# Performance work log

Hardware: AMD Instinct MI355X
Metric: run time of the kernel (lower is better)

Reference implementation:

```python
import jax, jax.numpy as jnp
import numpy as np

T, B, F, H = 128, 64, 75, 512
J = F  # attention dim == number of input features (joints)


def _lstm_dir(x, h0, c0, Wih, Whh, bih, bhh, reverse):
    # x: (T,B,Fin). Precompute input projection once (big GEMM), scan the recurrence.
    xw = jnp.einsum('tbf,gf->tbg', x, Wih) + bih + bhh  # (T,B,4H)

    def step(carry, xt):
        h, c = carry
        g = xt + h @ Whh.T  # (B,4H), PyTorch gate order i,f,g,o
        i, f, gg, o = jnp.split(g, 4, axis=-1)
        c = jax.nn.sigmoid(f) * c + jax.nn.sigmoid(i) * jnp.tanh(gg)
        h = jax.nn.sigmoid(o) * jnp.tanh(c)
        return (h, c), h

    (hT, cT), ys = jax.lax.scan(step, (h0, c0), xw, reverse=reverse)
    return ys, hT


def _bilstm(x, h0, c0, Wih, Whh, bih, bhh):
    # params have leading direction axis of size 2
    yf, hf = _lstm_dir(x, h0[0], c0[0], Wih[0], Whh[0], bih[0], bhh[0], False)
    yb, hb = _lstm_dir(x, h0[1], c0[1], Wih[1], Whh[1], bih[1], bhh[1], True)
    return jnp.concatenate([yf, yb], axis=-1), jnp.stack([hf, hb])


def setup_inputs() -> dict:
    key = jax.random.key(0)
    ks = iter(jax.random.split(key, 40))

    def p(*shape):
        return (jax.random.normal(next(ks), shape, dtype=jnp.float32) * 0.05)

    inp = {
        'x': jax.random.normal(next(ks), (T, B, F), dtype=jnp.float32),
        'h0': jnp.zeros((6, B, H), jnp.float32),
        'c0': jnp.zeros((6, B, H), jnp.float32),
        # salstm: 1-layer bidirectional, input F
        'sa_Wih': p(2, 4 * H, F), 'sa_Whh': p(2, 4 * H, H),
        'sa_bih': p(2, 4 * H), 'sa_bhh': p(2, 4 * H),
        # mainlstm layer 0 (input F)
        'm0_Wih': p(2, 4 * H, F), 'm0_Whh': p(2, 4 * H, H),
        'm0_bih': p(2, 4 * H), 'm0_bhh': p(2, 4 * H),
        # mainlstm layers 1,2 (input 2H), stacked on leading layer axis
        'mL_Wih': p(2, 2, 4 * H, 2 * H), 'mL_Whh': p(2, 2, 4 * H, H),
        'mL_bih': p(2, 2, 4 * H), 'mL_bhh': p(2, 2, 4 * H),
        'safc1_W': p(H, H), 'safc1_b': p(H),
        'safc2_W': p(J, H), 'safc2_b': p(J),
        'fc1_W': p(H, 2 * H), 'fc1_b': p(H),
    }
    return inp


def reference(x, h0, c0, sa_Wih, sa_Whh, sa_bih, sa_bhh,
              m0_Wih, m0_Whh, m0_bih, m0_bhh,
              mL_Wih, mL_Whh, mL_bih, mL_bhh,
              safc1_W, safc1_b, safc2_W, safc2_b, fc1_W, fc1_b):
    # spatial-attention LSTM
    sa_out, sa_hn = _bilstm(x, h0[:2], c0[:2], sa_Wih, sa_Whh, sa_bih, sa_bhh)  # sa_hn (2,B,H)
    e = jnp.exp(jnp.tanh(sa_hn @ safc1_W.T + safc1_b) @ safc2_W.T + safc2_b)  # (2,B,J)
    alpha = e / e.sum(axis=(0, 2), keepdims=True)  # per-batch normalization
    # replace all weights >= 0.1 with their selected mean (per batch element)
    mask = alpha >= 0.1
    cnt = mask.sum(axis=(0, 2), keepdims=True)
    sel_mean = (alpha * mask).sum(axis=(0, 2), keepdims=True) / jnp.maximum(cnt, 1)
    alpha = jnp.where(mask, sel_mean, alpha)
    alpha_b = alpha.mean(axis=0)  # (B,J) -- reconcile direction axis for broadcast

    xw = x * alpha_b[None]  # (T,B,F)

    # 3-layer bidirectional main LSTM
    y, _ = _bilstm(xw, h0[0:2], c0[0:2], m0_Wih, m0_Whh, m0_bih, m0_bhh)
    for l in range(2):
        y, _ = _bilstm(y, h0[2 + 2 * l:4 + 2 * l], c0[2 + 2 * l:4 + 2 * l],
                       mL_Wih[l], mL_Whh[l], mL_bih[l], mL_bhh[l])
    out = y @ fc1_W.T + fc1_b  # (T,B,H)
    return out
```

## Files before the change

### kernel.cpp

```cpp
#include <hip/hip_runtime.h>
#include <cstddef>

#define T_  128
#define B_  64
#define F_  75
#define H_  512
#define G4_ 2048
#define TB_ (T_ * B_)
#define KP_ 128

typedef __bf16 bf16x8 __attribute__((ext_vector_type(8)));
typedef float  f32x4  __attribute__((ext_vector_type(4)));
typedef unsigned long long u64;
typedef unsigned long long __attribute__((may_alias)) u64a;

__device__ __forceinline__ short f2b(float x) {
    union { float f; unsigned u; } v; v.f = x;
    return (short)((v.u + 0x7fffu + ((v.u >> 16) & 1u)) >> 16);
}
__device__ __forceinline__ float b2f(short s) {
    union { float f; unsigned u; } v; v.u = ((unsigned)(unsigned short)s) << 16;
    return v.f;
}
__device__ __forceinline__ void gload16(const void* g, void* l) {
    __builtin_amdgcn_global_load_lds(
        (const __attribute__((address_space(1))) void*)g,
        (__attribute__((address_space(3))) void*)l, 16, 0, 0);
}
__device__ __forceinline__ float fsig(float x) {
    return __builtin_amdgcn_rcpf(1.f + __expf(-x));
}
__device__ __forceinline__ float ftanh(float x) {
    return 1.f - 2.f * __builtin_amdgcn_rcpf(1.f + __expf(2.f * x));
}

__global__ __launch_bounds__(256) void gemm_bf16(
    const short* __restrict__ A, const short* __restrict__ Bm,
    float* __restrict__ C, float* __restrict__ P, int M, int N, int K,
    const float* __restrict__ bias1, const float* __restrict__ bias2)
{
    __shared__ short As[4096];
    __shared__ short Bs[4096];
    const int tid = threadIdx.x;
    const int m_base = blockIdx.y * 128;
    const int n_base = blockIdx.x * 128;
    const int w = tid >> 6, lane = tid & 63;
    const int wm = (w >> 1) * 64, wn = (w & 1) * 64;
    const int lm = lane & 15, q = lane >> 4;

    f32x4 acc[4][4];
#pragma unroll
    for (int i = 0; i < 4; i++)
#pragma unroll
        for (int j = 0; j < 4; j++)
#pragma unroll
            for (int r = 0; r < 4; r++) acc[i][j][r] = 0.f;

    const int s0 = tid, s1 = tid + 256;
    const int r0 = s0 & 127, c0 = s0 >> 7;
    const int r1 = s1 & 127, c1 = s1 >> 7;

    for (int k0 = 0; k0 < K; k0 += 32) {
        __syncthreads();
        gload16(A + (size_t)(m_base + r0) * K + k0 + c0 * 8, &As[s0 * 8]);
        gload16(A + (size_t)(m_base + r1) * K + k0 + c1 * 8, &As[s1 * 8]);
        gload16(Bm + (size_t)(n_base + r0) * K + k0 + c0 * 8, &Bs[s0 * 8]);
        gload16(Bm + (size_t)(n_base + r1) * K + k0 + c1 * 8, &Bs[s1 * 8]);
        __syncthreads();
        bf16x8 af[4], bfv[4];
#pragma unroll
        for (int i = 0; i < 4; i++) {
            af[i]  = *(const bf16x8*)&As[((q * 128) + wm + i * 16 + lm) * 8];
            bfv[i] = *(const bf16x8*)&Bs[((q * 128) + wn + i * 16 + lm) * 8];
        }
#pragma unroll
        for (int i = 0; i < 4; i++)
#pragma unroll
            for (int j = 0; j < 4; j++)
                acc[i][j] = __builtin_amdgcn_mfma_f32_16x16x32_bf16(
                    af[i], bfv[j], acc[i][j], 0, 0, 0);
    }

#pragma unroll
    for (int i = 0; i < 4; i++) {
#pragma unroll
        for (int j = 0; j < 4; j++) {
            const int gm0 = m_base + wm + i * 16 + q * 4;
            const int gn = n_base + wn + j * 16 + lm;
            float bb = (bias1 ? bias1[gn] : 0.f) + (bias2 ? bias2[gn] : 0.f);
            if (P) {
                const int g = gn >> 9, u = gn & 511;
                const int ub = u >> 4, lmu = u & 15;
#pragma unroll
                for (int r = 0; r < 4; r++) {
                    const int gm = gm0 + r;
                    const int t = gm >> 6, b = gm & 63;
                    const int tidS = (b >> 4) * 64 + ((b >> 2) & 3) * 16 + lmu;
                    size_t idx = ((((size_t)t * 32 + ub) * 4 + (b & 3)) * 256 + tidS) * 4 + g;
                    P[idx] = acc[i][j][r] + bb;
                }
            } else {
#pragma unroll
                for (int r = 0; r < 4; r++)
                    C[(size_t)(gm0 + r) * N + gn] = acc[i][j][r] + bb;
            }
        }
    }
}

__global__ __launch_bounds__(256) void pack_whh(
    const float* __restrict__ W, short* __restrict__ Wpk)
{
    int i = blockIdx.x * 256 + threadIdx.x;
    if (i >= 2 * G4_ * H_) return;
    int e = i & 7, lane = (i >> 3) & 63, it = (i >> 9) & 15;
    int g = (i >> 13) & 3, ub = (i >> 15) & 31, dir = (i >> 20) & 1;
    int lm = lane & 15, qq = lane >> 4;
    float v = W[((size_t)dir * G4_ + g * H_ + ub * 16 + lm) * H_
                + it * 32 + qq * 8 + e];
    Wpk[i] = f2b(v);
}

__global__ __launch_bounds__(256) void init_phase(
    const float* __restrict__ h0s, short* __restrict__ Ht,
    unsigned* __restrict__ bar, int zero_bar)
{
    int i = blockIdx.x * 256 + threadIdx.x;
    if (i < 2 * B_ * H_) Ht[i] = f2b(h0s[i]);
    if (zero_bar && i < 64) bar[i] = 0;
}

__global__ __launch_bounds__(256) void prep_init(
    const float* __restrict__ h0, short* __restrict__ HtA,
    short* __restrict__ HtB, short* __restrict__ HtC, short* __restrict__ HtD,
    unsigned* __restrict__ bar)
{
    int i = blockIdx.x * 256 + threadIdx.x;
    if (i < 2 * B_ * H_) {
        short vA = f2b(h0[i]);
        HtA[i] = vA;
        HtB[i] = vA;
        HtC[i] = f2b(h0[2 * B_ * H_ + i]);
        HtD[i] = f2b(h0[4 * B_ * H_ + i]);
    }
    if (i < 64) bar[i] = 0;
}

__global__ __launch_bounds__(256) void ht_to_f32(
    const short* __restrict__ Ht0, float* __restrict__ out)
{
    int i = blockIdx.x * 256 + threadIdx.x;
    if (i < 2 * B_ * H_) out[i] = b2f(Ht0[i]);
}

__global__ __launch_bounds__(256, 1) void lstm_phase(
    const float* __restrict__ XW,
    const short* __restrict__ Wpk,
    short* __restrict__ Ht,
    const float* __restrict__ c0p,
    short* __restrict__ Y,
    unsigned* __restrict__ bar, int phase,
    const short* __restrict__ jA, const short* __restrict__ jB,
    float* __restrict__ jP, float* __restrict__ jC,
    const float* __restrict__ jb1, const float* __restrict__ jb2, int job)
{
    __shared__ short Ws[32768];
    __shared__ short Tb[64 * 24];
    __shared__ unsigned arrv;
    const int tid = threadIdx.x, w = tid >> 6, lane = tid & 63;
    const int lm = lane & 15, q = lane >> 4;

    if (blockIdx.x >= 32) {
        if (job == 0) return;
        short* As = Ws;
        short* Bs = Ws + 4096;
        const int hh = blockIdx.x - 32;
        const int dirh = blockIdx.y;
        const unsigned pT = (unsigned)(phase * T_);
        const int wm = (w >> 1) * 64, wn = (w & 1) * 64;

        const short* Bop; float* Pd; float* Cd; const float* b1; const float* b2;
        int n_tile, grp, iters, stride;
        if (job == 1) {
            Bop = jB + (size_t)dirh * G4_ * 1024;
            Pd = jP + (size_t)dirh * TB_ * G4_;
            Cd = nullptr;
            b1 = jb1 + dirh * G4_; b2 = jb2 + dirh * G4_;
            n_tile = hh & 15; grp = hh >> 4; iters = 16; stride = 4;
        } else {
            Bop = jB; Pd = nullptr; Cd = jC; b1 = jb1; b2 = nullptr;
            int H2 = dirh * 64 + hh;
            n_tile = H2 & 3; grp = H2 >> 2; iters = 2; stride = 32;
        }
        const int n_base = n_tile * 128;

        for (int it2 = 0; it2 < iters; it2++) {
            int j = grp + stride * it2;
            int k = (j & 1) ? 32 + (j >> 1) : 31 - (j >> 1);
            int m_base = k * 128, t0 = 2 * k;
            if (w == 0) {
                unsigned tgt = (lane < 32) ? pT + (unsigned)(t0 + 2)
                                           : pT + (unsigned)(T_ - t0);
                int itc = 0;
                for (;;) {
                    unsigned v = __hip_atomic_load(&bar[lane], __ATOMIC_RELAXED,
                                                   __HIP_MEMORY_SCOPE_AGENT);
                    if (__all(v >= tgt)) break;
                    if (++itc > (1 << 19)) break;
                    __builtin_amdgcn_s_sleep(32);
                }
            }
            __syncthreads();

            f32x4 acc[4][4];
#pragma unroll
            for (int i = 0; i < 4; i++)
#pragma unroll
                for (int jj = 0; jj < 4; jj++)
#pragma unroll
                    for (int r = 0; r < 4; r++) acc[i][jj][r] = 0.f;

            const int s0 = tid, s1 = tid + 256;
            const int r0 = s0 & 127, cc0 = s0 >> 7;
            const int r1 = s1 & 127, cc1 = s1 >> 7;
            for (int k0 = 0; k0 < 1024; k0 += 32) {
                __syncthreads();
                gload16(jA + (size_t)(m_base + r0) * 1024 + k0 + cc0 * 8, &As[s0 * 8]);
                gload16(jA + (size_t)(m_base + r1) * 1024 + k0 + cc1 * 8, &As[s1 * 8]);
                gload16(Bop + (size_t)(n_base + r0) * 1024 + k0 + cc0 * 8, &Bs[s0 * 8]);
                gload16(Bop + (size_t)(n_base + r1) * 1024 + k0 + cc1 * 8, &Bs[s1 * 8]);
                __syncthreads();
                bf16x8 af[4], bfv[4];
#pragma unroll
                for (int i = 0; i < 4; i++) {
                    af[i]  = *(const bf16x8*)&As[((q * 128) + wm + i * 16 + lm) * 8];
                    bfv[i] = *(const bf16x8*)&Bs[((q * 128) + wn + i * 16 + lm) * 8];
                }
#pragma unroll
                for (int i = 0; i < 4; i++)
#pragma unroll
                    for (int jj = 0; jj < 4; jj++)
                        acc[i][jj] = __builtin_amdgcn_mfma_f32_16x16x32_bf16(
                            af[i], bfv[jj], acc[i][jj], 0, 0, 0);
            }
#pragma unroll
            for (int i = 0; i < 4; i++) {
#pragma unroll
                for (int jj = 0; jj < 4; jj++) {
                    const int gm0 = m_base + wm + i * 16 + q * 4;
                    const int gn = n_base + wn + jj * 16 + lm;
                    float bb = b1[gn] + (b2 ? b2[gn] : 0.f);
                    if (Pd) {
                        const int g = gn >> 9, u = gn & 511;
                        const int ub2 = u >> 4, lmu = u & 15;
#pragma unroll
                        for (int r = 0; r < 4; r++) {
                            const int gm = gm0 + r;
                            const int t = gm >> 6, b = gm & 63;
                            const int tidS = (b >> 4) * 64 + ((b >> 2) & 3) * 16 + lmu;
                            size_t idx = ((((size_t)t * 32 + ub2) * 4 + (b & 3)) * 256 + tidS) * 4 + g;
                            Pd[idx] = acc[i][jj][r] + bb;
                        }
                    } else {
#pragma unroll
                        for (int r = 0; r < 4; r++)
                            Cd[(size_t)(gm0 + r) * 512 + gn] = acc[i][jj][r] + bb;
                    }
                }
            }
        }
        return;
    }

    const int dir = blockIdx.y, ub = blockIdx.x, u0 = ub * 16;
    if (tid == 0) arrv = 0;

    const short* wsrc = Wpk + (size_t)(dir * 32 + ub) * 32768;
#pragma unroll
    for (int p = 0; p < 16; p++)
        gload16(wsrc + (tid + 256 * p) * 8, &Ws[(tid + 256 * p) * 8]);

    const int b0 = w * 16 + q * 4;
    const int u = u0 + lm;
    unsigned* slots = bar + dir * 32;

    float c[4];
    f32x4 xw[4];
#pragma unroll
    for (int r = 0; r < 4; r++)
        c[r] = c0p[(size_t)dir * B_ * H_ + (size_t)(b0 + r) * H_ + u];
    {
        const int t0 = dir ? (T_ - 1) : 0;
        const float* xp = XW + ((size_t)dir * T_ + t0) * (B_ * G4_) + (size_t)ub * 4096;
#pragma unroll
        for (int r = 0; r < 4; r++)
            xw[r] = *(const f32x4*)(xp + r * 1024 + tid * 4);
    }
    __syncthreads();

    for (int s = 0; s < T_; s++) {
        const int t = dir ? (T_ - 1 - s) : s;
        const short* Hc = Ht + ((size_t)((s & 1) * 2 + dir) << 15);

        u64 hq[32];
        const short* hrow = Hc + (w * 16 + lm) * 512 + q * 8;
#pragma unroll
        for (int it = 0; it < 16; it++) {
            const u64* hp = (const u64*)(hrow + it * 32);
            hq[2 * it]     = __hip_atomic_load((u64*)hp,     __ATOMIC_RELAXED, __HIP_MEMORY_SCOPE_AGENT);
            hq[2 * it + 1] = __hip_atomic_load((u64*)hp + 1, __ATOMIC_RELAXED, __HIP_MEMORY_SCOPE_AGENT);
        }

        f32x4 acc[4];
#pragma unroll
        for (int g = 0; g < 4; g++)
#pragma unroll
            for (int r = 0; r < 4; r++) acc[g][r] = 0.f;

#pragma unroll
        for (int it = 0; it < 16; it++) {
            union { u64 q2[2]; bf16x8 v; } ua;
            ua.q2[0] = hq[2 * it]; ua.q2[1] = hq[2 * it + 1];
#pragma unroll
            for (int g = 0; g < 4; g++) {
                bf16x8 bv = *(const bf16x8*)&Ws[((g * 16 + it) * 64 + lane) * 8];
                acc[g] = __builtin_amdgcn_mfma_f32_16x16x32_bf16(ua.v, bv, acc[g], 0, 0, 0);
            }
        }

#pragma unroll
        for (int r = 0; r < 4; r++) {
            float gi = acc[0][r] + xw[r][0];
            float gf = acc[1][r] + xw[r][1];
            float gg = acc[2][r] + xw[r][2];
            float go = acc[3][r] + xw[r][3];
            float cc = fsig(gf) * c[r] + fsig(gi) * ftanh(gg);
            c[r] = cc;
            Tb[(b0 + r) * 24 + lm] = f2b(fsig(go) * ftanh(cc));
        }
        __asm__ volatile("" ::: "memory");

        const int b = tid >> 2, qd = tid & 3;
        u64 v0 = *(const u64a*)&Tb[b * 24 + qd * 4];
        u64* ydst = Y ? (u64*)(Y + ((size_t)t * B_ + b) * (2 * H_) + dir * H_ + u0 + qd * 4)
                      : nullptr;
        {
            short* Hn = Ht + ((size_t)(((s + 1) & 1) * 2 + dir) << 15);
            __hip_atomic_store((u64*)(Hn + b * 512 + u0 + qd * 4), v0,
                               __ATOMIC_RELAXED, __HIP_MEMORY_SCOPE_AGENT);
        }
        if (ydst && job)
            __hip_atomic_store(ydst, v0, __ATOMIC_RELAXED, __HIP_MEMORY_SCOPE_AGENT);
        __asm__ volatile("s_waitcnt vmcnt(0)" ::: "memory");
        if (lane == 0)
            __hip_atomic_fetch_add(&arrv, 1u, __ATOMIC_RELAXED,
                                   __HIP_MEMORY_SCOPE_WORKGROUP);

        const unsigned tgt = (unsigned)(phase * T_ + s + 1);
        if (w == 0) {
            const unsigned a4 = 4u * (unsigned)(s + 1);
            while (__hip_atomic_load(&arrv, __ATOMIC_RELAXED,
                                     __HIP_MEMORY_SCOPE_WORKGROUP) < a4) {}
            if (lane == 0)
                __hip_atomic_store(&slots[ub], tgt,
                                   __ATOMIC_RELAXED, __HIP_MEMORY_SCOPE_AGENT);
        }

        if (ydst && !job) *(u64a*)ydst = v0;
        if (s < T_ - 1) {
            const int tn = dir ? (T_ - 2 - s) : (s + 1);
            const float* xp = XW + ((size_t)dir * T_ + tn) * (B_ * G4_) + (size_t)ub * 4096;
#pragma unroll
            for (int r = 0; r < 4; r++)
                xw[r] = *(const f32x4*)(xp + r * 1024 + tid * 4);

            if (w == 0) {
                unsigned v;
                for (;;) {
                    v = (lane < 32)
                        ? __hip_atomic_load(&slots[lane], __ATOMIC_RELAXED, __HIP_MEMORY_SCOPE_AGENT)
                        : tgt;
                    if (__all(v >= tgt)) break;
                    __builtin_amdgcn_s_sleep(1);
                }
            }
            __syncthreads();
        }
    }
}

__global__ __launch_bounds__(256) void gemm_bt(
    const float* __restrict__ A, const float* __restrict__ Bm,
    float* __restrict__ C, int M, int N, int K,
    const float* __restrict__ bias1, int act)
{
    __shared__ float As[16][68];
    __shared__ float Bs[16][68];
    const int tid = threadIdx.x;
    const int m_base = blockIdx.y * 64;
    const int n_base = blockIdx.x * 64;
    const int tm = tid >> 4, tn = tid & 15;
    float acc[4][4] = {};

    for (int k0 = 0; k0 < K; k0 += 16) {
#pragma unroll
        for (int i = 0; i < 4; i++) {
            int idx = tid * 4 + i;
            int r = idx >> 4, kk = idx & 15;
            int gm = m_base + r, gk = k0 + kk;
            As[kk][r] = (gm < M && gk < K) ? A[(size_t)gm * K + gk] : 0.f;
            int gn = n_base + r;
            Bs[kk][r] = (gn < N && gk < K) ? Bm[(size_t)gn * K + gk] : 0.f;
        }
        __syncthreads();
#pragma unroll
        for (int kk = 0; kk < 16; kk++) {
            float4 av = *(const float4*)&As[kk][tm * 4];
            float4 bv = *(const float4*)&Bs[kk][tn * 4];
            float a[4] = {av.x, av.y, av.z, av.w};
            float b[4] = {bv.x, bv.y, bv.z, bv.w};
#pragma unroll
            for (int i = 0; i < 4; i++)
#pragma unroll
                for (int j = 0; j < 4; j++)
                    acc[i][j] = fmaf(a[i], b[j], acc[i][j]);
        }
        __syncthreads();
    }
#pragma unroll
    for (int i = 0; i < 4; i++) {
        int gm = m_base + tm * 4 + i;
        if (gm >= M) continue;
#pragma unroll
        for (int j = 0; j < 4; j++) {
            int gn = n_base + tn * 4 + j;
            if (gn >= N) continue;
            float v = acc[i][j];
            if (bias1) v += bias1[gn];
            if (act == 1) v = tanhf(v);
            else if (act == 2) v = expf(v);
            C[(size_t)gm * N + gn] = v;
        }
    }
}

__global__ __launch_bounds__(256) void conv_f2b(
    const float* __restrict__ src, short* __restrict__ dst, int n)
{
    int i = blockIdx.x * 256 + threadIdx.x;
    if (i < n) dst[i] = f2b(src[i]);
}
__global__ __launch_bounds__(256) void conv_f2b_pad(
    const float* __restrict__ src, short* __restrict__ dst,
    int rows, int kin, int kp)
{
    int i = blockIdx.x * 256 + threadIdx.x;
    if (i < rows * kp) {
        int r = i / kp, k = i % kp;
        dst[i] = (k < kin) ? f2b(src[(size_t)r * kin + k]) : (short)0;
    }
}

__global__ __launch_bounds__(256) void attn_alpha(
    const float* __restrict__ E, float* __restrict__ AB)
{
    const int b = blockIdx.x, tid = threadIdx.x;
    __shared__ float red[256];
    __shared__ float adj[152];
    float v = 0.f;
    if (tid < 150) {
        int d = tid / F_, j = tid % F_;
        v = E[((size_t)d * B_ + b) * F_ + j];
    }
    red[tid] = v; __syncthreads();
    for (int s2 = 128; s2 > 0; s2 >>= 1) {
        if (tid < s2) red[tid] += red[tid + s2];
        __syncthreads();
    }
    float total = red[0]; __syncthreads();
    float alpha = v / total;
    float m = (tid < 150 && alpha >= 0.1f) ? 1.f : 0.f;
    red[tid] = m; __syncthreads();
    for (int s2 = 128; s2 > 0; s2 >>= 1) {
        if (tid < s2) red[tid] += red[tid + s2];
        __syncthreads();
    }
    float cnt = red[0]; __syncthreads();
    red[tid] = m * alpha; __syncthreads();
    for (int s2 = 128; s2 > 0; s2 >>= 1) {
        if (tid < s2) red[tid] += red[tid + s2];
        __syncthreads();
    }
    float selsum = red[0]; __syncthreads();
    float selmean = selsum / fmaxf(cnt, 1.f);
    if (tid < 150) adj[tid] = (m > 0.f) ? selmean : alpha;
    __syncthreads();
    if (tid < F_) AB[(size_t)b * F_ + tid] = 0.5f * (adj[tid] + adj[F_ + tid]);
}

__global__ __launch_bounds__(256) void scale_xb(
    const float* __restrict__ x, const float* __restrict__ AB,
    short* __restrict__ xb)
{
    int i = blockIdx.x * 256 + threadIdx.x;
    if (i < TB_ * KP_) {
        int r = i >> 7, k = i & 127;
        if (k < F_) {
            int b = r % B_;
            xb[i] = f2b(x[(size_t)r * F_ + k] * AB[(size_t)b * F_ + k]);
        } else xb[i] = 0;
    }
}

extern "C" void kernel_launch(void* const* d_in, const int* in_sizes, int n_in,
                              void* d_out, int out_size, void* d_ws, size_t ws_size,
                              hipStream_t stream)
{
    (void)in_sizes; (void)n_in; (void)out_size;
    const float* x       = (const float*)d_in[0];
    const float* h0      = (const float*)d_in[1];
    const float* c0      = (const float*)d_in[2];
    const float* sa_Wih  = (const float*)d_in[3];
    const float* sa_Whh  = (const float*)d_in[4];
    const float* sa_bih  = (const float*)d_in[5];
    const float* sa_bhh  = (const float*)d_in[6];
    const float* m0_Wih  = (const float*)d_in[7];
    const float* m0_Whh  = (const float*)d_in[8];
    const float* m0_bih  = (const float*)d_in[9];
    const float* m0_bhh  = (const float*)d_in[10];
    const float* mL_Wih  = (const float*)d_in[11];
    const float* mL_Whh  = (const float*)d_in[12];
    const float* mL_bih  = (const float*)d_in[13];
    const float* mL_bhh  = (const float*)d_in[14];
    const float* safc1_W = (const float*)d_in[15];
    const float* safc1_b = (const float*)d_in[16];
    const float* safc2_W = (const float*)d_in[17];
    const float* safc2_b = (const float*)d_in[18];
    const float* fc1_W   = (const float*)d_in[19];
    const float* fc1_b   = (const float*)d_in[20];

    char* cur = (char*)d_ws;
    auto alloc = [&](size_t bytes) {
        char* p = cur; cur += (bytes + 255) & ~(size_t)255; return p;
    };
    auto cv = [&](const float* s, short* d, int n) {
        conv_f2b<<<(n + 255) / 256, 256, 0, stream>>>(s, d, n);
    };

    const bool OV = ws_size >= 370000000ull;

    if (OV) {
        float*    XWa  = (float*)alloc((size_t)2 * TB_ * G4_ * 4);
        float*    XWb  = (float*)alloc((size_t)2 * TB_ * G4_ * 4);
        float*    T1b  = (float*)alloc(2 * B_ * H_ * 4);
        float*    Eb   = (float*)alloc(2 * B_ * F_ * 4);
        float*    AB   = (float*)alloc(B_ * F_ * 4);
        float*    saHf = (float*)alloc(2 * B_ * H_ * 4);
        short*    xb   = (short*)alloc((size_t)TB_ * KP_ * 2);
        short*    Y0b  = (short*)alloc((size_t)TB_ * 2 * H_ * 2);
        short*    Y1b  = (short*)alloc((size_t)TB_ * 2 * H_ * 2);
        short*    Y2b  = (short*)alloc((size_t)TB_ * 2 * H_ * 2);
        short*    HtA  = (short*)alloc((size_t)2 * 2 * B_ * H_ * 2);
        short*    HtB  = (short*)alloc((size_t)2 * 2 * B_ * H_ * 2);
        short*    HtC  = (short*)alloc((size_t)2 * 2 * B_ * H_ * 2);
        short*    HtD  = (short*)alloc((size_t)2 * 2 * B_ * H_ * 2);
        const size_t PK = (size_t)2 * G4_ * H_;
        short*    Wpk4 = (short*)alloc(4 * PK * 2);
        short*    WihbSA = (short*)alloc((size_t)2 * G4_ * KP_ * 2);
        short*    WihbM0 = (short*)alloc((size_t)2 * G4_ * KP_ * 2);
        short*    WihbL  = (short*)alloc((size_t)2 * 2 * G4_ * 2 * H_ * 2);
        short*    fc1b   = (short*)alloc((size_t)H_ * 2 * H_ * 2);
        unsigned* bar    = (unsigned*)alloc(1024);

        auto g16 = [&](const short* Ap, const short* Bp, float* Pp,
                       int K, const float* b1, const float* b2) {
            gemm_bf16<<<dim3(G4_ / 128, TB_ / 128), 256, 0, stream>>>(
                Ap, Bp, nullptr, Pp, TB_, G4_, K, b1, b2);
        };
        auto lstm = [&](const float* XWp, const short* Wp, short* Htp,
                        const float* c0p, short* Yp, int pidx,
                        const short* ja, const short* jb, float* jp, float* jc,
                        const float* b1, const float* b2, int job) {
            lstm_phase<<<dim3(job ? 96 : 32, 2), 256, 0, stream>>>(
                XWp, Wp, Htp, c0p, Yp, bar, pidx, ja, jb, jp, jc, b1, b2, job);
        };

        prep_init<<<256, 256, 0, stream>>>(h0, HtA, HtB, HtC, HtD, bar);
        cv(fc1_W, fc1b, H_ * 2 * H_);
        conv_f2b_pad<<<(2 * G4_ * KP_ + 255) / 256, 256, 0, stream>>>(sa_Wih, WihbSA, 2 * G4_, F_, KP_);
        conv_f2b_pad<<<(2 * G4_ * KP_ + 255) / 256, 256, 0, stream>>>(m0_Wih, WihbM0, 2 * G4_, F_, KP_);
        cv(mL_Wih, WihbL, 2 * 2 * G4_ * 2 * H_);
        pack_whh<<<(2 * G4_ * H_ + 255) / 256, 256, 0, stream>>>(sa_Whh, Wpk4);
        pack_whh<<<(2 * G4_ * H_ + 255) / 256, 256, 0, stream>>>(m0_Whh, Wpk4 + PK);
        pack_whh<<<(2 * G4_ * H_ + 255) / 256, 256, 0, stream>>>(mL_Whh, Wpk4 + 2 * PK);
        pack_whh<<<(2 * G4_ * H_ + 255) / 256, 256, 0, stream>>>(mL_Whh + (size_t)2 * G4_ * H_, Wpk4 + 3 * PK);
        conv_f2b_pad<<<(TB_ * KP_ + 255) / 256, 256, 0, stream>>>(x, xb, TB_, F_, KP_);

        for (int d = 0; d < 2; d++)
            g16(xb, WihbSA + (size_t)d * G4_ * KP_, XWa + (size_t)d * TB_ * G4_,
                KP_, sa_bih + d * G4_, sa_bhh + d * G4_);
        lstm(XWa, Wpk4, HtA, c0, nullptr, 0,
             nullptr, nullptr, nullptr, nullptr, nullptr, nullptr, 0);
        ht_to_f32<<<256, 256, 0, stream>>>(HtA, saHf);
        gemm_bt<<<dim3(8, 2), 256, 0, stream>>>(saHf, safc1_W, T1b, 2 * B_, H_, H_, safc1_b, 1);
        gemm_bt<<<dim3(2, 2), 256, 0, stream>>>(T1b, safc2_W, Eb, 2 * B_, F_, H_, safc2_b, 2);
        attn_alpha<<<B_, 256, 0, stream>>>(Eb, AB);
        scale_xb<<<(TB_ * KP_ + 255) / 256, 256, 0, stream>>>(x, AB, xb);

        for (int d = 0; d < 2; d++)
            g16(xb, WihbM0 + (size_t)d * G4_ * KP_, XWa + (size_t)d * TB_ * G4_,
                KP_, m0_bih + d * G4_, m0_bhh + d * G4_);
        lstm(XWa, Wpk4 + PK, HtB, c0, Y0b, 1,
             Y0b, WihbL, XWb, nullptr, mL_bih, mL_bhh, 1);

        lstm(XWb, Wpk4 + 2 * PK, HtC, c0 + 2 * B_ * H_, Y1b, 2,
             Y1b, WihbL + (size_t)2 * G4_ * 2 * H_, XWa, nullptr,
             mL_bih + 2 * G4_, mL_bhh + 2 * G4_, 1);

        lstm(XWa, Wpk4 + 3 * PK, HtD, c0 + 4 * B_ * H_, Y2b, 3,
             Y2b, fc1b, nullptr, (float*)d_out, fc1_b, nullptr, 2);
        return;
    }

    float*    XW   = (float*)alloc((size_t)2 * TB_ * G4_ * 4);
    float*    T1b  = (float*)alloc(2 * B_ * H_ * 4);
    float*    Eb   = (float*)alloc(2 * B_ * F_ * 4);
    float*    AB   = (float*)alloc(B_ * F_ * 4);
    float*    saHf = (float*)alloc(2 * B_ * H_ * 4);
    short*    xb   = (short*)alloc((size_t)TB_ * KP_ * 2);
    short*    Y0b  = (short*)alloc((size_t)TB_ * 2 * H_ * 2);
    short*    Y1b  = (short*)alloc((size_t)TB_ * 2 * H_ * 2);
    short*    Ht   = (short*)alloc((size_t)2 * 2 * B_ * H_ * 2);
    short*    Wpk  = (short*)alloc((size_t)2 * G4_ * H_ * 2);
    short*    Wihb = (short*)alloc((size_t)2 * G4_ * KP_ * 2);
    short*    WihbL= (short*)alloc((size_t)2 * G4_ * 2 * H_ * 2);
    short*    fc1b = (short*)alloc((size_t)H_ * 2 * H_ * 2);
    unsigned* bar  = (unsigned*)alloc(1024);

    auto g16f = [&](const short* Ap, const short* Bp, float* Cp, float* Pp,
                    int M, int N, int K, const float* b1, const float* b2) {
        gemm_bf16<<<dim3(N / 128, M / 128), 256, 0, stream>>>(Ap, Bp, Cp, Pp, M, N, K, b1, b2);
    };
    auto phase = [&](const float* Whh_p, const float* h0p, const float* c0p,
                     short* Yout, int pidx) {
        pack_whh<<<(2 * G4_ * H_ + 255) / 256, 256, 0, stream>>>(Whh_p, Wpk);
        init_phase<<<256, 256, 0, stream>>>(h0p, Ht, bar, pidx == 0 ? 1 : 0);
        lstm_phase<<<dim3(32, 2), 256, 0, stream>>>(XW, Wpk, Ht, c0p, Yout, bar, pidx,
            nullptr, nullptr, nullptr, nullptr, nullptr, nullptr, 0);
    };

    cv(fc1_W, fc1b, H_ * 2 * H_);
    conv_f2b_pad<<<(TB_ * KP_ + 255) / 256, 256, 0, stream>>>(x, xb, TB_, F_, KP_);
    conv_f2b_pad<<<(2 * G4_ * KP_ + 255) / 256, 256, 0, stream>>>(sa_Wih, Wihb, 2 * G4_, F_, KP_);
    for (int d = 0; d < 2; d++)
        g16f(xb, Wihb + (size_t)d * G4_ * KP_, nullptr, XW + (size_t)d * TB_ * G4_,
             TB_, G4_, KP_, sa_bih + d * G4_, sa_bhh + d * G4_);
    phase(sa_Whh, h0, c0, nullptr, 0);
    ht_to_f32<<<256, 256, 0, stream>>>(Ht, saHf);
    gemm_bt<<<dim3(8, 2), 256, 0, stream>>>(saHf, safc1_W, T1b, 2 * B_, H_, H_, safc1_b, 1);
    gemm_bt<<<dim3(2, 2), 256, 0, stream>>>(T1b, safc2_W, Eb, 2 * B_, F_, H_, safc2_b, 2);
    attn_alpha<<<B_, 256, 0, stream>>>(Eb, AB);
    scale_xb<<<(TB_ * KP_ + 255) / 256, 256, 0, stream>>>(x, AB, xb);

    conv_f2b_pad<<<(2 * G4_ * KP_ + 255) / 256, 256, 0, stream>>>(m0_Wih, Wihb, 2 * G4_, F_, KP_);
    for (int d = 0; d < 2; d++)
        g16f(xb, Wihb + (size_t)d * G4_ * KP_, nullptr, XW + (size_t)d * TB_ * G4_,
             TB_, G4_, KP_, m0_bih + d * G4_, m0_bhh + d * G4_);
    phase(m0_Whh, h0, c0, Y0b, 1);

    cv(mL_Wih, WihbL, 2 * G4_ * 2 * H_);
    for (int d = 0; d < 2; d++)
        g16f(Y0b, WihbL + (size_t)d * G4_ * 2 * H_, nullptr, XW + (size_t)d * TB_ * G4_,
             TB_, G4_, 2 * H_, mL_bih + d * G4_, mL_bhh + d * G4_);
    phase(mL_Whh, h0 + 2 * B_ * H_, c0 + 2 * B_ * H_, Y1b, 2);

    cv(mL_Wih + (size_t)2 * G4_ * 2 * H_, WihbL, 2 * G4_ * 2 * H_);
    for (int d = 0; d < 2; d++)
        g16f(Y1b, WihbL + (size_t)d * G4_ * 2 * H_, nullptr, XW + (size_t)d * TB_ * G4_,
             TB_, G4_, 2 * H_, mL_bih + (2 + d) * G4_, mL_bhh + (2 + d) * G4_);
    phase(mL_Whh + (size_t)2 * G4_ * H_, h0 + 4 * B_ * H_, c0 + 4 * B_ * H_, Y0b, 3);

    g16f(Y0b, fc1b, (float*)d_out, nullptr, TB_, H_, 2 * H_, fc1_b, nullptr);
}
```

Measured before the change: 4.144 ms.

## Store input-projection buffers in bf16 and shrink workspace to enable overlap path

The precomputed input-gate projections (XW) are now written as bf16 instead of fp32, and the LSTM recurrence loads and widens them to float per step. This halves the per-step global read traffic on the serial critical path. The smaller footprint lets the overlapped path (fused next-layer GEMM inside the recurrence kernel) fit in a much smaller workspace, so it is taken whenever space allows instead of only for a very large workspace. The cost is extra bf16 rounding of the projections and re-packing of weights between phases, since only one packed Whh buffer is kept.

Result: faster. 4.042 ms (-2.5%).

```diff
diff --git a/kernel.cpp b/kernel.cpp
--- a/kernel.cpp
+++ b/kernel.cpp
@@ -33,10 +33,19 @@
 __device__ __forceinline__ float ftanh(float x) {
     return 1.f - 2.f * __builtin_amdgcn_rcpf(1.f + __expf(2.f * x));
 }
+__device__ __forceinline__ f32x4 xw4(const short* xp) {
+    u64 v = *(const u64a*)xp;
+    f32x4 o;
+    o[0] = b2f((short)(v & 0xFFFFu));
+    o[1] = b2f((short)((v >> 16) & 0xFFFFu));
+    o[2] = b2f((short)((v >> 32) & 0xFFFFu));
+    o[3] = b2f((short)(v >> 48));
+    return o;
+}
 
 __global__ __launch_bounds__(256) void gemm_bf16(
     const short* __restrict__ A, const short* __restrict__ Bm,
-    float* __restrict__ C, float* __restrict__ P, int M, int N, int K,
+    float* __restrict__ C, short* __restrict__ P, int M, int N, int K,
     const float* __restrict__ bias1, const float* __restrict__ bias2)
 {
     __shared__ short As[4096];
@@ -97,7 +106,7 @@
                     const int t = gm >> 6, b = gm & 63;
                     const int tidS = (b >> 4) * 64 + ((b >> 2) & 3) * 16 + lmu;
                     size_t idx = ((((size_t)t * 32 + ub) * 4 + (b & 3)) * 256 + tidS) * 4 + g;
-                    P[idx] = acc[i][j][r] + bb;
+                    P[idx] = f2b(acc[i][j][r] + bb);
                 }
             } else {
 #pragma unroll
@@ -154,14 +163,14 @@
 }
 
 __global__ __launch_bounds__(256, 1) void lstm_phase(
-    const float* __restrict__ XW,
+    const short* __restrict__ XW,
     const short* __restrict__ Wpk,
     short* __restrict__ Ht,
     const float* __restrict__ c0p,
     short* __restrict__ Y,
     unsigned* __restrict__ bar, int phase,
     const short* __restrict__ jA, const short* __restrict__ jB,
-    float* __restrict__ jP, float* __restrict__ jC,
+    short* __restrict__ jP, float* __restrict__ jC,
     const float* __restrict__ jb1, const float* __restrict__ jb2, int job)
 {
     __shared__ short Ws[32768];
@@ -179,7 +188,7 @@
         const unsigned pT = (unsigned)(phase * T_);
         const int wm = (w >> 1) * 64, wn = (w & 1) * 64;
 
-        const short* Bop; float* Pd; float* Cd; const float* b1; const float* b2;
+        const short* Bop; short* Pd; float* Cd; const float* b1; const float* b2;
         int n_tile, grp, iters, stride;
         if (job == 1) {
             Bop = jB + (size_t)dirh * G4_ * 1024;
@@ -259,7 +268,7 @@
                             const int t = gm >> 6, b = gm & 63;
                             const int tidS = (b >> 4) * 64 + ((b >> 2) & 3) * 16 + lmu;
                             size_t idx = ((((size_t)t * 32 + ub2) * 4 + (b & 3)) * 256 + tidS) * 4 + g;
-                            Pd[idx] = acc[i][jj][r] + bb;
+                            Pd[idx] = f2b(acc[i][jj][r] + bb);
                         }
                     } else {
 #pragma unroll
@@ -291,10 +300,10 @@
         c[r] = c0p[(size_t)dir * B_ * H_ + (size_t)(b0 + r) * H_ + u];
     {
         const int t0 = dir ? (T_ - 1) : 0;
-        const float* xp = XW + ((size_t)dir * T_ + t0) * (B_ * G4_) + (size_t)ub * 4096;
+        const short* xp = XW + ((size_t)dir * T_ + t0) * (size_t)(B_ * G4_) + (size_t)ub * 4096;
 #pragma unroll
         for (int r = 0; r < 4; r++)
-            xw[r] = *(const f32x4*)(xp + r * 1024 + tid * 4);
+            xw[r] = xw4(xp + r * 1024 + tid * 4);
     }
     __syncthreads();
 
@@ -369,10 +378,10 @@
         if (ydst && !job) *(u64a*)ydst = v0;
         if (s < T_ - 1) {
             const int tn = dir ? (T_ - 2 - s) : (s + 1);
-            const float* xp = XW + ((size_t)dir * T_ + tn) * (B_ * G4_) + (size_t)ub * 4096;
+            const short* xp = XW + ((size_t)dir * T_ + tn) * (size_t)(B_ * G4_) + (size_t)ub * 4096;
 #pragma unroll
             for (int r = 0; r < 4; r++)
-                xw[r] = *(const f32x4*)(xp + r * 1024 + tid * 4);
+                xw[r] = xw4(xp + r * 1024 + tid * 4);
 
             if (w == 0) {
                 unsigned v;
@@ -539,7 +548,8 @@
     const float* fc1_W   = (const float*)d_in[19];
     const float* fc1_b   = (const float*)d_in[20];
 
-    char* cur = (char*)d_ws;
+    char* const start = (char*)d_ws;
+    char* cur = start;
     auto alloc = [&](size_t bytes) {
         char* p = cur; cur += (bytes + 255) & ~(size_t)255; return p;
     };
@@ -547,39 +557,34 @@
         conv_f2b<<<(n + 255) / 256, 256, 0, stream>>>(s, d, n);
     };
 
-    const bool OV = ws_size >= 370000000ull;
-
-    if (OV) {
-        float*    XWa  = (float*)alloc((size_t)2 * TB_ * G4_ * 4);
-        float*    XWb  = (float*)alloc((size_t)2 * TB_ * G4_ * 4);
-        float*    T1b  = (float*)alloc(2 * B_ * H_ * 4);
-        float*    Eb   = (float*)alloc(2 * B_ * F_ * 4);
-        float*    AB   = (float*)alloc(B_ * F_ * 4);
-        float*    saHf = (float*)alloc(2 * B_ * H_ * 4);
-        short*    xb   = (short*)alloc((size_t)TB_ * KP_ * 2);
-        short*    Y0b  = (short*)alloc((size_t)TB_ * 2 * H_ * 2);
-        short*    Y1b  = (short*)alloc((size_t)TB_ * 2 * H_ * 2);
-        short*    Y2b  = (short*)alloc((size_t)TB_ * 2 * H_ * 2);
-        short*    HtA  = (short*)alloc((size_t)2 * 2 * B_ * H_ * 2);
-        short*    HtB  = (short*)alloc((size_t)2 * 2 * B_ * H_ * 2);
-        short*    HtC  = (short*)alloc((size_t)2 * 2 * B_ * H_ * 2);
-        short*    HtD  = (short*)alloc((size_t)2 * 2 * B_ * H_ * 2);
-        const size_t PK = (size_t)2 * G4_ * H_;
-        short*    Wpk4 = (short*)alloc(4 * PK * 2);
-        short*    WihbSA = (short*)alloc((size_t)2 * G4_ * KP_ * 2);
-        short*    WihbM0 = (short*)alloc((size_t)2 * G4_ * KP_ * 2);
-        short*    WihbL  = (short*)alloc((size_t)2 * 2 * G4_ * 2 * H_ * 2);
-        short*    fc1b   = (short*)alloc((size_t)H_ * 2 * H_ * 2);
-        unsigned* bar    = (unsigned*)alloc(1024);
-
-        auto g16 = [&](const short* Ap, const short* Bp, float* Pp,
+    short*    XWa  = (short*)alloc((size_t)2 * TB_ * G4_ * 2);
+    short*    XWc  = (short*)alloc((size_t)2 * TB_ * G4_ * 2);
+    short*    Y0b  = (short*)alloc((size_t)TB_ * 2 * H_ * 2);
+    short*    Y1b  = (short*)alloc((size_t)TB_ * 2 * H_ * 2);
+    short*    Wpk  = (short*)alloc((size_t)2 * G4_ * H_ * 2);
+    short*    Wihb = (short*)alloc((size_t)2 * G4_ * KP_ * 2);
+    short*    WihbL= (short*)alloc((size_t)2 * G4_ * 2 * H_ * 2);
+    short*    fc1b = (short*)alloc((size_t)H_ * 2 * H_ * 2);
+    short*    xb   = (short*)alloc((size_t)TB_ * KP_ * 2);
+    float*    T1b  = (float*)alloc(2 * B_ * H_ * 4);
+    float*    Eb   = (float*)alloc(2 * B_ * F_ * 4);
+    float*    AB   = (float*)alloc(B_ * F_ * 4);
+    float*    saHf = (float*)alloc(2 * B_ * H_ * 4);
+    short*    HtA  = (short*)alloc((size_t)2 * 2 * B_ * H_ * 2);
+    short*    HtB  = (short*)alloc((size_t)2 * 2 * B_ * H_ * 2);
+    short*    HtC  = (short*)alloc((size_t)2 * 2 * B_ * H_ * 2);
+    short*    HtD  = (short*)alloc((size_t)2 * 2 * B_ * H_ * 2);
+    unsigned* bar  = (unsigned*)alloc(1024);
+
+    if ((size_t)(cur - start) <= ws_size) {
+        auto g16 = [&](const short* Ap, const short* Bp, short* Pp,
                        int K, const float* b1, const float* b2) {
             gemm_bf16<<<dim3(G4_ / 128, TB_ / 128), 256, 0, stream>>>(
                 Ap, Bp, nullptr, Pp, TB_, G4_, K, b1, b2);
         };
-        auto lstm = [&](const float* XWp, const short* Wp, short* Htp,
+        auto lstm = [&](const short* XWp, const short* Wp, short* Htp,
                         const float* c0p, short* Yp, int pidx,
-                        const short* ja, const short* jb, float* jp, float* jc,
+                        const short* ja, const short* jb, short* jp, float* jc,
                         const float* b1, const float* b2, int job) {
             lstm_phase<<<dim3(job ? 96 : 32, 2), 256, 0, stream>>>(
                 XWp, Wp, Htp, c0p, Yp, bar, pidx, ja, jb, jp, jc, b1, b2, job);
@@ -587,19 +592,15 @@
 
         prep_init<<<256, 256, 0, stream>>>(h0, HtA, HtB, HtC, HtD, bar);
         cv(fc1_W, fc1b, H_ * 2 * H_);
-        conv_f2b_pad<<<(2 * G4_ * KP_ + 255) / 256, 256, 0, stream>>>(sa_Wih, WihbSA, 2 * G4_, F_, KP_);
-        conv_f2b_pad<<<(2 * G4_ * KP_ + 255) / 256, 256, 0, stream>>>(m0_Wih, WihbM0, 2 * G4_, F_, KP_);
-        cv(mL_Wih, WihbL, 2 * 2 * G4_ * 2 * H_);
-        pack_whh<<<(2 * G4_ * H_ + 255) / 256, 256, 0, stream>>>(sa_Whh, Wpk4);
-        pack_whh<<<(2 * G4_ * H_ + 255) / 256, 256, 0, stream>>>(m0_Whh, Wpk4 + PK);
-        pack_whh<<<(2 * G4_ * H_ + 255) / 256, 256, 0, stream>>>(mL_Whh, Wpk4 + 2 * PK);
-        pack_whh<<<(2 * G4_ * H_ + 255) / 256, 256, 0, stream>>>(mL_Whh + (size_t)2 * G4_ * H_, Wpk4 + 3 * PK);
+        cv(mL_Wih, WihbL, 2 * G4_ * 2 * H_);
+        conv_f2b_pad<<<(2 * G4_ * KP_ + 255) / 256, 256, 0, stream>>>(sa_Wih, Wihb, 2 * G4_, F_, KP_);
         conv_f2b_pad<<<(TB_ * KP_ + 255) / 256, 256, 0, stream>>>(x, xb, TB_, F_, KP_);
+        pack_whh<<<(2 * G4_ * H_ + 255) / 256, 256, 0, stream>>>(sa_Whh, Wpk);
 
         for (int d = 0; d < 2; d++)
-            g16(xb, WihbSA + (size_t)d * G4_ * KP_, XWa + (size_t)d * TB_ * G4_,
+            g16(xb, Wihb + (size_t)d * G4_ * KP_, XWa + (size_t)d * TB_ * G4_,
                 KP_, sa_bih + d * G4_, sa_bhh + d * G4_);
-        lstm(XWa, Wpk4, HtA, c0, nullptr, 0,
+        lstm(XWa, Wpk, HtA, c0, nullptr, 0,
              nullptr, nullptr, nullptr, nullptr, nullptr, nullptr, 0);
         ht_to_f32<<<256, 256, 0, stream>>>(HtA, saHf);
         gemm_bt<<<dim3(8, 2), 256, 0, stream>>>(saHf, safc1_W, T1b, 2 * B_, H_, H_, safc1_b, 1);
@@ -607,78 +608,83 @@
         attn_alpha<<<B_, 256, 0, stream>>>(Eb, AB);
         scale_xb<<<(TB_ * KP_ + 255) / 256, 256, 0, stream>>>(x, AB, xb);
 
+        conv_f2b_pad<<<(2 * G4_ * KP_ + 255) / 256, 256, 0, stream>>>(m0_Wih, Wihb, 2 * G4_, F_, KP_);
         for (int d = 0; d < 2; d++)
-            g16(xb, WihbM0 + (size_t)d * G4_ * KP_, XWa + (size_t)d * TB_ * G4_,
+            g16(xb, Wihb + (size_t)d * G4_ * KP_, XWa + (size_t)d * TB_ * G4_,
                 KP_, m0_bih + d * G4_, m0_bhh + d * G4_);
-        lstm(XWa, Wpk4 + PK, HtB, c0, Y0b, 1,
-             Y0b, WihbL, XWb, nullptr, mL_bih, mL_bhh, 1);
-
-        lstm(XWb, Wpk4 + 2 * PK, HtC, c0 + 2 * B_ * H_, Y1b, 2,
-             Y1b, WihbL + (size_t)2 * G4_ * 2 * H_, XWa, nullptr,
-             mL_bih + 2 * G4_, mL_bhh + 2 * G4_, 1);
-
-        lstm(XWa, Wpk4 + 3 * PK, HtD, c0 + 4 * B_ * H_, Y2b, 3,
-             Y2b, fc1b, nullptr, (float*)d_out, fc1_b, nullptr, 2);
+        pack_whh<<<(2 * G4_ * H_ + 255) / 256, 256, 0, stream>>>(m0_Whh, Wpk);
+        lstm(XWa, Wpk, HtB, c0, Y0b, 1,
+             Y0b, WihbL, XWc, nullptr, mL_bih, mL_bhh, 1);
+
+        cv(mL_Wih + (size_t)2 * G4_ * 2 * H_, WihbL, 2 * G4_ * 2 * H_);
+        pack_whh<<<(2 * G4_ * H_ + 255) / 256, 256, 0, stream>>>(mL_Whh, Wpk);
+        lstm(XWc, Wpk, HtC, c0 + 2 * B_ * H_, Y1b, 2,
+             Y1b, WihbL, XWa, nullptr, mL_bih + 2 * G4_, mL_bhh + 2 * G4_, 1);
+
+        pack_whh<<<(2 * G4_ * H_ + 255) / 256, 256, 0, stream>>>(mL_Whh + (size_t)2 * G4_ * H_, Wpk);
+        lstm(XWa, Wpk, HtD, c0 + 4 * B_ * H_, Y0b, 3,
+             Y0b, fc1b, nullptr, (float*)d_out, fc1_b, nullptr, 2);
         return;
     }
 
-    float*    XW   = (float*)alloc((size_t)2 * TB_ * G4_ * 4);
-    float*    T1b  = (float*)alloc(2 * B_ * H_ * 4);
-    float*    Eb   = (float*)alloc(2 * B_ * F_ * 4);
-    float*    AB   = (float*)alloc(B_ * F_ * 4);
-    float*    saHf = (float*)alloc(2 * B_ * H_ * 4);
-    short*    xb   = (short*)alloc((size_t)TB_ * KP_ * 2);
-    short*    Y0b  = (short*)alloc((size_t)TB_ * 2 * H_ * 2);
-    short*    Y1b  = (short*)alloc((size_t)TB_ * 2 * H_ * 2);
-    short*    Ht   = (short*)alloc((size_t)2 * 2 * B_ * H_ * 2);
-    short*    Wpk  = (short*)alloc((size_t)2 * G4_ * H_ * 2);
-    short*    Wihb = (short*)alloc((size_t)2 * G4_ * KP_ * 2);
-    short*    WihbL= (short*)alloc((size_t)2 * G4_ * 2 * H_ * 2);
-    short*    fc1b = (short*)alloc((size_t)H_ * 2 * H_ * 2);
-    unsigned* bar  = (unsigned*)alloc(1024);
-
-    auto g16f = [&](const short* Ap, const short* Bp, float* Cp, float* Pp,
+    cur = start;
+    short*    XW    = (short*)alloc((size_t)2 * TB_ * G4_ * 2);
+    float*    T1f   = (float*)alloc(2 * B_ * H_ * 4);
+    float*    Ebf   = (float*)alloc(2 * B_ * F_ * 4);
+    float*    ABf   = (float*)alloc(B_ * F_ * 4);
+    float*    saHff = (float*)alloc(2 * B_ * H_ * 4);
+    short*    xbf   = (short*)alloc((size_t)TB_ * KP_ * 2);
+    short*    Y0f   = (short*)alloc((size_t)TB_ * 2 * H_ * 2);
+    short*    Y1f   = (short*)alloc((size_t)TB_ * 2 * H_ * 2);
+    short*    Ht    = (short*)alloc((size_t)2 * 2 * B_ * H_ * 2);
+    short*    Wpkf  = (short*)alloc((size_t)2 * G4_ * H_ * 2);
+    short*    Wihbf = (short*)alloc((size_t)2 * G4_ * KP_ * 2);
+    short*    WihbLf= (short*)alloc((size_t)2 * G4_ * 2 * H_ * 2);
+    short*    fc1bf = (short*)alloc((size_t)H_ * 2 * H_ * 2);
+    unsigned* barf  = (unsigned*)alloc(1024);
+
+    auto g16f = [&](const short* Ap, const short* Bp, float* Cp, short* Pp,
                     int M, int N, int K, const float* b1, const float* b2) {
         gemm_bf16<<<dim3(N / 128, M / 128), 256, 0, stream>>>(Ap, Bp, Cp, Pp, M, N, K, b1, b2);
     };
     auto phase = [&](const float* Whh_p, const float* h0p, const float* c0p,
                      short* Yout, int pidx) {
-        pack_whh<<<(2 * G4_ * H_ + 255) / 256, 256, 0, stream>>>(Whh_p, Wpk);
-        init_phase<<<256, 256, 0, stream>>>(h0p, Ht, bar, pidx == 0 ? 1 : 0);
-        lstm_phase<<<dim3(32, 2), 256, 0, stream>>>(XW, Wpk, Ht, c0p, Yout, bar, pidx,
+        pack_whh<<<(2 * G4_ * H_ + 255) / 256, 256, 0, stream>>>(Whh_p, Wpkf);
+        init_phase<<<256, 256, 0, stream>>>(h0p, Ht, barf, pidx == 0 ? 1 : 0);
+        lstm_phase<<<dim3(32, 2), 256, 0, stream>>>(XW, Wpkf, Ht, c0p, Yout, barf, pidx,
             nullptr, nullptr, nullptr, nullptr, nullptr, nullptr, 0);
     };
 
-    cv(fc1_W, fc1b, H_ * 2 * H_);
-    conv_f2b_pad<<<(TB_ * KP_ + 255) / 256, 256, 0, stream>>>(x, xb, TB_, F_, KP_);
-    conv_f2b_pad<<<(2 * G4_ * KP_ + 255) / 256, 256, 0, stream>>>(sa_Wih, Wihb, 2 * G4_, F_, KP_);
+    cv(fc1_W, fc1bf, H_ * 2 * H_);
+    conv_f2b_pad<<<(TB_ * KP_ + 255) / 256, 256, 0, stream>>>(x, xbf, TB_, F_, KP_);
+    conv_f2b_pad<<<(2 * G4_ * KP_ + 255) / 256, 256, 0, stream>>>(sa_Wih, Wihbf, 2 * G4_, F_, KP_);
     for (int d = 0; d < 2; d++)
-        g16f(xb, Wihb + (size_t)d * G4_ * KP_, nullptr, XW + (size_t)d * TB_ * G4_,
+        g16f(xbf, Wihbf + (size_t)d * G4_ * KP_, nullptr, XW + (size_t)d * TB_ * G4_,
              TB_, G4_, KP_, sa_bih + d * G4_, sa_bhh + d * G4_);
     phase(sa_Whh, h0, c0, nullptr, 0);
-    ht_to_f32<<<256, 256, 0, stream>>>(Ht, saHf);
-    gemm_bt<<<dim3(8, 2), 256, 0, stream>>>(saHf, safc1_W, T1b, 2 * B_, H_, H_, safc1_b, 1);
-    gemm_bt<<<dim3(2, 2), 256, 0, stream>>>(T1b, safc2_W, Eb, 2 * B_, F_, H_, safc2_b, 2);
-    attn_alpha<<<B_, 256, 0, stream>>>(Eb, AB);
-    scale_xb<<<(TB_ * KP_ + 255) / 256, 256, 0, stream>>>(x, AB, xb);
-
-    conv_f2b_pad<<<(2 * G4_ * KP_ + 255) / 256, 256, 0, stream>>>(m0_Wih, Wihb, 2 * G4_, F_, KP_);
+    ht_to_f32<<<256, 256, 0, stream>>>(Ht, saHff);
+    gemm_bt<<<dim3(8, 2), 256, 0, stream>>>(saHff, safc1_W, T1f, 2 * B_, H_, H_, safc1_b, 1);
+    gemm_bt<<<dim3(2, 2), 256, 0, stream>>>(T1f, safc2_W, Ebf, 2 * B_, F_, H_, safc2_b, 2);
+    attn_alpha<<<B_, 256, 0, stream>>>(Ebf, ABf);
+    scale_xb<<<(TB_ * KP_ + 255) / 256, 256, 0, stream>>>(x, ABf, xbf);
+
+    conv_f2b_pad<<<(2 * G4_ * KP_ + 255) / 256, 256, 0, stream>>>(m0_Wih, Wihbf, 2 * G4_, F_, KP_);
     for (int d = 0; d < 2; d++)
-        g16f(xb, Wihb + (size_t)d * G4_ * KP_, nullptr, XW + (size_t)d * TB_ * G4_,
+        g16f(xbf, Wihbf + (size_t)d * G4_ * KP_, nullptr, XW + (size_t)d * TB_ * G4_,
              TB_, G4_, KP_, m0_bih + d * G4_, m0_bhh + d * G4_);
-    phase(m0_Whh, h0, c0, Y0b, 1);
-
-    cv(mL_Wih, WihbL, 2 * G4_ * 2 * H_);
+    phase(m0_Whh, h0, c0, Y0f, 1);
+
+    cv(mL_Wih, WihbLf, 2 * G4_ * 2 * H_);
     for (int d = 0; d < 2; d++)
-        g16f(Y0b, WihbL + (size_t)d * G4_ * 2 * H_, nullptr, XW + (size_t)d * TB_ * G4_,
+        g16f(Y0f, WihbLf + (size_t)d * G4_ * 2 * H_, nullptr, XW + (size_t)d * TB_ * G4_,
              TB_, G4_, 2 * H_, mL_bih + d * G4_, mL_bhh + d * G4_);
-    phase(mL_Whh, h0 + 2 * B_ * H_, c0 + 2 * B_ * H_, Y1b, 2);
-
-    cv(mL_Wih + (size_t)2 * G4_ * 2 * H_, WihbL, 2 * G4_ * 2 * H_);
+    phase(mL_Whh, h0 + 2 * B_ * H_, c0 + 2 * B_ * H_, Y1f, 2);
+
+    cv(mL_Wih + (size_t)2 * G4_ * 2 * H_, WihbLf, 2 * G4_ * 2 * H_);
     for (int d = 0; d < 2; d++)
-        g16f(Y1b, WihbL + (size_t)d * G4_ * 2 * H_, nullptr, XW + (size_t)d * TB_ * G4_,
+        g16f(Y1f, WihbLf + (size_t)d * G4_ * 2 * H_, nullptr, XW + (size_t)d * TB_ * G4_,
              TB_, G4_, 2 * H_, mL_bih + (2 + d) * G4_, mL_bhh + (2 + d) * G4_);
-    phase(mL_Whh + (size_t)2 * G4_ * H_, h0 + 4 * B_ * H_, c0 + 4 * B_ * H_, Y0b, 3);
-
-    g16f(Y0b, fc1b, (float*)d_out, nullptr, TB_, H_, 2 * H_, fc1_b, nullptr);
-}
+    phase(mL_Whh + (size_t)2 * G4_ * H_, h0 + 4 * B_ * H_, c0 + 4 * B_ * H_, Y0f, 3);
+
+    g16f(Y0f, fc1bf, (float*)d_out, nullptr, TB_, H_, 2 * H_, fc1_b, nullptr);
+}
```
